# Optimization experiments

Hardware: AMD Instinct MI355X
Metric: run time of the kernel (lower is better)

## Reference

```python
import jax, jax.numpy as jnp
import numpy as np

N_NODES = 32768
N_EDGES = 196608
N_GRAPHS = 256
DEG = 6
HID = 128
RVD = 16
EMB = HID - RVD   # atom/bond embedding dim = hidden - random_vec_dim
VOCAB = 128
TGT = 256
DEPTH = 5
N_AGG = 4         # mean, max, min, std
N_SC = 3          # identity, amplification, attenuation
EPS = 1e-5


def setup_inputs() -> dict:
    key = jax.random.key(0)
    ks = jax.random.split(key, 12)

    def g(i, shape, scale=0.05):
        return jax.random.normal(ks[i], shape, dtype=jnp.float32) * scale

    return {
        "atom_feats": jax.random.randint(ks[0], (N_NODES, 9), 0, 100),
        "bond_feats": jax.random.randint(ks[1], (N_EDGES, 3), 0, 4),
        "src": jax.random.randint(ks[2], (N_EDGES,), 0, N_NODES),
        # every node receives exactly DEG messages (DGL reduce requires in-edges)
        "dst": jnp.repeat(jnp.arange(N_NODES), DEG),
        "graph_ids": jnp.repeat(jnp.arange(N_GRAPHS), N_NODES // N_GRAPHS),
        "n_graphs": N_GRAPHS,
        "rand_x": jax.random.normal(ks[3], (N_NODES, RVD), dtype=jnp.float32),   # std=1.0
        "rand_edge": jax.random.normal(ks[4], (N_EDGES, RVD), dtype=jnp.float32),
        "atom_emb": g(5, (9, VOCAB, EMB)),
        "bond_emb": g(6, (3, VOCAB, EMB)),
        "pre_W": g(7, (DEPTH, 3 * HID, HID)),
        "pre_b": jnp.zeros((DEPTH, HID), jnp.float32),
        "post_W": g(8, (DEPTH, (N_AGG * N_SC + 1) * HID, HID)),
        "post_b": jnp.zeros((DEPTH, HID), jnp.float32),
        "ro_W1": g(9, (3 * HID, HID)),
        "ro_b1": jnp.zeros((HID,), jnp.float32),
        "ro_W2": g(10, (HID, TGT)),
        "ro_b2": jnp.zeros((TGT,), jnp.float32),
    }


def reference(atom_feats, bond_feats, src, dst, graph_ids, n_graphs,
              rand_x, rand_edge, atom_emb, bond_emb,
              pre_W, pre_b, post_W, post_b, ro_W1, ro_b1, ro_W2, ro_b2):
    n = atom_feats.shape[0]
    # OGB-style encoders: sum of per-column embeddings, then concat random vec
    h = jnp.concatenate([atom_emb[jnp.arange(9), atom_feats].sum(1), rand_x], -1)   # [N, HID]
    ef = jnp.concatenate([bond_emb[jnp.arange(3), bond_feats].sum(1), rand_edge], -1)  # [E, HID]

    deg = jax.ops.segment_sum(jnp.ones((dst.shape[0],), h.dtype), dst, n)
    degc = jnp.maximum(deg, 1.0)[:, None]
    logD = jnp.log(deg + 1.0)[:, None]                 # avg_d['log'] = 1.0
    inv_logD = jnp.where(logD > 0, 1.0 / jnp.maximum(logD, EPS), 0.0)

    def layer(hc, p):
        pW, pb, qW, qb = p
        # pretrans MLP on [src_feat, dst_feat, edge_feat]; last_activation = activation (relu)
        z = jnp.concatenate([hc[src], hc[dst], ef], -1)          # [E, 3*HID]
        e = jax.nn.relu(z @ pW + pb)                             # [E, HID]
        s = jax.ops.segment_sum(e, dst, n)
        mean = s / degc
        mean_sq = jax.ops.segment_sum(e * e, dst, n) / degc
        mx = jax.ops.segment_max(e, dst, n)
        mn = jax.ops.segment_min(e, dst, n)
        std = jnp.sqrt(jax.nn.relu(mean_sq - mean * mean) + EPS)
        agg = jnp.concatenate([mean, mx, mn, std], -1)           # [N, 4*HID]
        scaled = jnp.concatenate([agg, agg * logD, agg * inv_logD], -1)  # [N, 12*HID]
        h_new = jnp.concatenate([hc, scaled], -1) @ qW + qb + hc  # posttrans (linear) + residual
        return h_new, None

    h, _ = jax.lax.scan(layer, h, (pre_W, pre_b, post_W, post_b))

    # multi-aggregator readout: mean, sum, max per graph
    cnt = jnp.maximum(jax.ops.segment_sum(jnp.ones((n,), h.dtype), graph_ids, n_graphs), 1.0)[:, None]
    gsum = jax.ops.segment_sum(h, graph_ids, n_graphs)
    gmax = jax.ops.segment_max(h, graph_ids, n_graphs)
    r = jnp.concatenate([gsum / cnt, gsum, gmax], -1)            # [G, 3*HID]
    return jax.nn.relu(r @ ro_W1 + ro_b1) @ ro_W2 + ro_b2        # [G, TGT]
```

## Files before the change

kernel.cpp:

```cpp
#include <hip/hip_runtime.h>
#include <hip/hip_bf16.h>

#define N_NODES 32768
#define N_EDGES 196608
#define N_GRAPHS 256
#define DEG 6
#define HID 128
#define RVD 16
#define EMB 112
#define VOCAB 128
#define TGT 256
#define DEPTH 5

#define LOG7 1.9459101090932196f
#define ILOG7 0.5138983423697507f

typedef __hip_bfloat16 bf16;
using frag_ab = __attribute__((ext_vector_type(8))) short;
using frag_cd = __attribute__((ext_vector_type(4))) float;
typedef float f32x2 __attribute__((ext_vector_type(2)));

static __device__ __forceinline__ float b2f(bf16 x) { return __bfloat162float(x); }
static __device__ __forceinline__ bf16  f2b(float x) { return __float2bfloat16(x); }
static __device__ __forceinline__ float us2f(unsigned short u) {
    unsigned int x = ((unsigned int)u) << 16;
    return __uint_as_float(x);
}
static __device__ __forceinline__ unsigned short f2us(float x) {
    bf16 b = __float2bfloat16(x);
    return *reinterpret_cast<unsigned short*>(&b);
}

#define PB_ENC  16384
#define PB_WB   (PB_ENC + 640)
#define PB_WC   (PB_WB + 1600)
#define PB_WR   (PB_WC + 80)
#define PB_CODE (PB_WR + 768)
#define PB_T    (PB_CODE + 320)

__global__ __launch_bounds__(256) void prep_k(const int* __restrict__ af, const float* __restrict__ rx,
                                              const float* __restrict__ aemb, bf16* __restrict__ h,
                                              const float* __restrict__ preW, const float* __restrict__ preB,
                                              const float* __restrict__ postW,
                                              const int* __restrict__ bfeat, const float* __restrict__ bemb,
                                              bf16* __restrict__ wb, bf16* __restrict__ wc,
                                              bf16* __restrict__ wrB, unsigned char* __restrict__ codeA,
                                              bf16* __restrict__ Tb) {
    int blk = blockIdx.x, tid = threadIdx.x;
    if (blk < PB_ENC) {
        int v = blk * 2 + (tid >> 7), c = tid & 127;
        float val;
        if (c < EMB) {
            val = 0.f;
            #pragma unroll
            for (int i = 0; i < 9; ++i) {
                int f = af[v * 9 + i];
                val += aemb[(i * VOCAB + f) * EMB + c];
            }
        } else {
            val = rx[v * RVD + (c - EMB)];
        }
        h[(size_t)v * HID + c] = f2b(val);
    } else if (blk < PB_WB) {
        int idx = (blk - PB_ENC) * 256 + tid;
        if (idx < DEPTH * 32768) {
            int j = idx & 7, L = (idx >> 3) & 63, nt = (idx >> 9) & 15, ks = (idx >> 13) & 3, l = idx >> 15;
            int k = ks * 32 + ((L >> 4) * 8) + j;
            int n = nt * 16 + (L & 15);
            const float* W = preW + (size_t)l * 384 * 128;
            float v = (n < 128) ? W[k * 128 + n] : W[(128 + k) * 128 + (n - 128)];
            wb[idx] = f2b(v);
        }
    } else if (blk < PB_WC) {
        int idx = (blk - PB_WB) * 256 + tid;
        if (idx < DEPTH * 81920) {
            int j = idx & 7, L = (idx >> 3) & 63, nt = (idx >> 9) & 7;
            int t = idx >> 12;
            int ks = t % 20, l = t / 20;
            int k = ks * 32 + ((L >> 4) * 8) + j;
            int n = nt * 16 + (L & 15);
            const float* W = postW + (size_t)l * 1664 * 128;
            float v;
            if (k < 128) {
                v = W[k * 128 + n];
            } else {
                int jj = k - 128;
                v = W[(128 + jj) * 128 + n] + LOG7 * W[(640 + jj) * 128 + n] + ILOG7 * W[(1152 + jj) * 128 + n];
            }
            wc[idx] = f2b(v);
        }
    } else if (blk < PB_WR) {
        int idx = (blk - PB_WC) * 256 + tid;
        if (idx < DEPTH * 4096) {
            int j = idx & 7, L = (idx >> 3) & 63, nt = (idx >> 9) & 7, l = idx >> 12;
            int k = ((L >> 4) * 8) + j;
            int n = nt * 16 + (L & 15);
            float v = (k < 16) ? preW[(size_t)l * 384 * 128 + (368 + k) * 128 + n] : 0.f;
            wrB[idx] = f2b(v);
        }
    } else if (blk < PB_CODE) {
        int e = (blk - PB_WR) * 256 + tid;
        if (e < N_EDGES)
            codeA[e] = (unsigned char)(bfeat[e * 3] | (bfeat[e * 3 + 1] << 2) | (bfeat[e * 3 + 2] << 4));
    } else {
        if (tid < 128) {
            int t = blk - PB_CODE;
            int l = t >> 6, cd = t & 63, c = tid;
            int f0 = cd & 3, f1 = (cd >> 2) & 3, f2 = cd >> 4;
            const float* W = preW + (size_t)l * 384 * 128 + 256 * 128;
            float acc = preB[l * 128 + c];
            #pragma unroll 4
            for (int k = 0; k < EMB; ++k) {
                float bsk = bemb[(0 * VOCAB + f0) * EMB + k]
                          + bemb[(1 * VOCAB + f1) * EMB + k]
                          + bemb[(2 * VOCAB + f2) * EMB + k];
                acc += bsk * W[k * 128 + c];
            }
            Tb[(size_t)(l * 64 + cd) * 128 + c] = f2b(acc);
        }
    }
}

__global__ __launch_bounds__(256) void gemm_z12(const bf16* __restrict__ A,
                                                const bf16* __restrict__ Bp,
                                                bf16* __restrict__ C) {
    int lane = threadIdx.x & 63;
    int wave = threadIdx.x >> 6;
    int m = lane & 15, quad = lane >> 4;
    int row0 = blockIdx.x * 64 + wave * 16;

    frag_cd acc[16];
    #pragma unroll
    for (int nt = 0; nt < 16; ++nt)
        #pragma unroll
        for (int i = 0; i < 4; ++i) acc[nt][i] = 0.f;

    const frag_ab* Bf = (const frag_ab*)Bp;
    const bf16* arow = A + (size_t)(row0 + m) * 128;
    #pragma unroll
    for (int ks = 0; ks < 4; ++ks) {
        frag_ab a = *(const frag_ab*)(arow + ks * 32 + quad * 8);
        #pragma unroll
        for (int nt = 0; nt < 16; ++nt) {
            frag_ab b = Bf[(ks * 16 + nt) * 64 + lane];
            acc[nt] = __builtin_amdgcn_mfma_f32_16x16x32_bf16(a, b, acc[nt], 0, 0, 0);
        }
    }
    #pragma unroll
    for (int nt = 0; nt < 16; ++nt) {
        int col = nt * 16 + m;
        #pragma unroll
        for (int r = 0; r < 4; ++r) {
            int row = row0 + quad * 4 + r;
            C[(size_t)row * 256 + col] = f2b(acc[nt][r]);
        }
    }
}

__global__ __launch_bounds__(512, 4) void fused_layer(bf16* __restrict__ h,
                                                      const bf16* __restrict__ Zcur,
                                                      const int* __restrict__ src,
                                                      const unsigned char* __restrict__ code,
                                                      const float* __restrict__ rand_edge,
                                                      const bf16* __restrict__ Tb,
                                                      const float* __restrict__ Wr,
                                                      const bf16* __restrict__ Bp,
                                                      const float* __restrict__ bias,
                                                      const bf16* __restrict__ Bn,
                                                      bf16* __restrict__ Znext) {
    __shared__ __align__(16) bf16 agg_lds[64 * 520];
    __shared__ __align__(16) float relds[8][384];

    int tid = threadIdx.x;
    int lane = tid & 63, wave = tid >> 6;
    int m = lane & 15, quad = lane >> 4;
    int row0 = blockIdx.x * 64;

    const unsigned short* Zu = (const unsigned short*)Zcur;
    const unsigned short* Tu = (const unsigned short*)Tb;
    unsigned short* Ag = (unsigned short*)agg_lds;
    int c = lane * 2;

    {
        const int vbase = row0 + wave * 8;

        f32x2 wr2[16];
        #pragma unroll
        for (int k = 0; k < 16; ++k) {
            float2 w2 = *(const float2*)(Wr + k * 128 + c);
            wr2[k].x = w2.x; wr2[k].y = w2.y;
        }

        {
            const float2* rb = (const float2*)(rand_edge + (size_t)vbase * 96);
            float2 a0 = rb[lane], a1 = rb[lane + 64], a2 = rb[lane + 128];
            float2* rl = (float2*)relds[wave];
            rl[lane] = a0; rl[lane + 64] = a1; rl[lane + 128] = a2;
        }
        float2 rh0, rh1, rh2;

        int svs[2][6]; int cds[2][6];
        ushort2 z1u[2][6], tvu[2][6], z2u[2];

        {
            const int2* sp = (const int2*)(src + vbase * 6);
            int2 a = sp[0], b = sp[1], d = sp[2];
            svs[0][0] = a.x; svs[0][1] = a.y; svs[0][2] = b.x;
            svs[0][3] = b.y; svs[0][4] = d.x; svs[0][5] = d.y;
            const unsigned short* cp = (const unsigned short*)(code + vbase * 6);
            unsigned short x = cp[0], y = cp[1], z = cp[2];
            cds[0][0] = x & 255; cds[0][1] = x >> 8; cds[0][2] = y & 255;
            cds[0][3] = y >> 8;  cds[0][4] = z & 255; cds[0][5] = z >> 8;
        }
        z2u[0] = *(const ushort2*)(Zu + (size_t)vbase * 256 + 128 + c);
        #pragma unroll
        for (int j = 0; j < 6; ++j) z1u[0][j] = *(const ushort2*)(Zu + (size_t)svs[0][j] * 256 + c);
        #pragma unroll
        for (int j = 0; j < 6; ++j) tvu[0][j] = *(const ushort2*)(Tu + cds[0][j] * 128 + c);
        {
            const int2* sp = (const int2*)(src + (vbase + 1) * 6);
            int2 a = sp[0], b = sp[1], d = sp[2];
            svs[1][0] = a.x; svs[1][1] = a.y; svs[1][2] = b.x;
            svs[1][3] = b.y; svs[1][4] = d.x; svs[1][5] = d.y;
            const unsigned short* cp = (const unsigned short*)(code + (vbase + 1) * 6);
            unsigned short x = cp[0], y = cp[1], z = cp[2];
            cds[1][0] = x & 255; cds[1][1] = x >> 8; cds[1][2] = y & 255;
            cds[1][3] = y >> 8;  cds[1][4] = z & 255; cds[1][5] = z >> 8;
        }

        #pragma unroll
        for (int i = 0; i < 8; ++i) {
            const int s = i & 1, t = s ^ 1;
            if (i == 2) {
                const float2* rb2 = (const float2*)(rand_edge + (size_t)(vbase + 4) * 96);
                rh0 = rb2[lane]; rh1 = rb2[lane + 64]; rh2 = rb2[lane + 128];
            }
            if (i == 4) {
                float2* rl = (float2*)relds[wave];
                rl[lane] = rh0; rl[lane + 64] = rh1; rl[lane + 128] = rh2;
            }
            if (i < 7) {
                z2u[t] = *(const ushort2*)(Zu + (size_t)(vbase + i + 1) * 256 + 128 + c);
                #pragma unroll
                for (int j = 0; j < 6; ++j) z1u[t][j] = *(const ushort2*)(Zu + (size_t)svs[t][j] * 256 + c);
                #pragma unroll
                for (int j = 0; j < 6; ++j) tvu[t][j] = *(const ushort2*)(Tu + cds[t][j] * 128 + c);
            }
            if (i < 6) {
                const int2* sp = (const int2*)(src + (vbase + i + 2) * 6);
                int2 a = sp[0], b = sp[1], d = sp[2];
                svs[s][0] = a.x; svs[s][1] = a.y; svs[s][2] = b.x;
                svs[s][3] = b.y; svs[s][4] = d.x; svs[s][5] = d.y;
                const unsigned short* cp = (const unsigned short*)(code + (vbase + i + 2) * 6);
                unsigned short x = cp[0], y = cp[1], z = cp[2];
                cds[s][0] = x & 255; cds[s][1] = x >> 8; cds[s][2] = y & 255;
                cds[s][3] = y >> 8;  cds[s][4] = z & 255; cds[s][5] = z >> 8;
            }

            float z2a = us2f(z2u[s].x), z2b = us2f(z2u[s].y);
            f32x2 s2  = {0.f, 0.f}, ss2 = {0.f, 0.f};
            f32x2 mx2 = {-1e30f, -1e30f}, mn2 = {1e30f, 1e30f};
            #pragma unroll
            for (int j = 0; j < 6; ++j) {
                const float4* rp = (const float4*)&relds[wave][(i & 3) * 96 + j * 16];
                float4 r0 = rp[0], r1 = rp[1], r2 = rp[2], r3 = rp[3];
                f32x2 v2;
                v2.x = us2f(z1u[s][j].x) + z2a + us2f(tvu[s][j].x);
                v2.y = us2f(z1u[s][j].y) + z2b + us2f(tvu[s][j].y);
                float rk[16] = {r0.x, r0.y, r0.z, r0.w, r1.x, r1.y, r1.z, r1.w,
                                r2.x, r2.y, r2.z, r2.w, r3.x, r3.y, r3.z, r3.w};
                #pragma unroll
                for (int k = 0; k < 16; ++k) v2 += rk[k] * wr2[k];
                v2 = __builtin_elementwise_max(v2, (f32x2){0.f, 0.f});
                s2 += v2;
                ss2 += v2 * v2;
                mx2 = __builtin_elementwise_max(mx2, v2);
                mn2 = __builtin_elementwise_min(mn2, v2);
            }
            f32x2 mean2 = s2 * (1.f / 6.f);
            f32x2 msq2  = ss2 * (1.f / 6.f);
            f32x2 var2  = __builtin_elementwise_max(msq2 - mean2 * mean2, (f32x2){0.f, 0.f});
            float sda = sqrtf(var2.x + 1e-5f), sdb = sqrtf(var2.y + 1e-5f);
            int lrow = wave * 8 + i;
            size_t base = (size_t)lrow * 520 + c;
            *(ushort2*)(Ag + base)       = make_ushort2(f2us(mean2.x), f2us(mean2.y));
            *(ushort2*)(Ag + base + 128) = make_ushort2(f2us(mx2.x),   f2us(mx2.y));
            *(ushort2*)(Ag + base + 256) = make_ushort2(f2us(mn2.x),   f2us(mn2.y));
            *(ushort2*)(Ag + base + 384) = make_ushort2(f2us(sda),     f2us(sdb));
        }
    }
    __syncthreads();

    int rt = wave & 3, nh = wave >> 2;
    int rowA = row0 + rt * 16 + m;

    frag_cd acc[4];
    #pragma unroll
    for (int nt = 0; nt < 4; ++nt)
        #pragma unroll
        for (int i = 0; i < 4; ++i) acc[nt][i] = 0.f;

    const frag_ab* Bf = (const frag_ab*)Bp;
    const bf16* arow = h + (size_t)rowA * 128;
    #pragma unroll
    for (int ks = 0; ks < 4; ++ks) {
        frag_ab a = *(const frag_ab*)(arow + ks * 32 + quad * 8);
        #pragma unroll
        for (int nt = 0; nt < 4; ++nt) {
            frag_ab b = Bf[(ks * 8 + nh * 4 + nt) * 64 + lane];
            acc[nt] = __builtin_amdgcn_mfma_f32_16x16x32_bf16(a, b, acc[nt], 0, 0, 0);
        }
    }
    const bf16* grow = agg_lds + (size_t)(rt * 16 + m) * 520;
    #pragma unroll
    for (int ks = 0; ks < 16; ++ks) {
        frag_ab a = *(const frag_ab*)(grow + ks * 32 + quad * 8);
        #pragma unroll
        for (int nt = 0; nt < 4; ++nt) {
            frag_ab b = Bf[((4 + ks) * 8 + nh * 4 + nt) * 64 + lane];
            acc[nt] = __builtin_amdgcn_mfma_f32_16x16x32_bf16(a, b, acc[nt], 0, 0, 0);
        }
    }

    __syncthreads();

    bf16* newh = agg_lds;
    #pragma unroll
    for (int nt = 0; nt < 4; ++nt) {
        int col = nh * 64 + nt * 16 + m;
        float bs_ = bias[col];
        #pragma unroll
        for (int r2 = 0; r2 < 4; ++r2) {
            int lr = rt * 16 + quad * 4 + r2;
            int row = row0 + lr;
            float nv = acc[nt][r2] + bs_ + b2f(h[(size_t)row * HID + col]);
            bf16 bv2 = f2b(nv);
            h[(size_t)row * HID + col] = bv2;
            newh[lr * 136 + col] = bv2;
        }
    }

    if (Bn) {
        __syncthreads();
        const frag_ab* Bf2 = (const frag_ab*)Bn;
        frag_cd a2[8];
        #pragma unroll
        for (int nt = 0; nt < 8; ++nt)
            #pragma unroll
            for (int i = 0; i < 4; ++i) a2[nt][i] = 0.f;
        #pragma unroll
        for (int ks = 0; ks < 4; ++ks) {
            frag_ab a = *(const frag_ab*)&newh[(rt * 16 + m) * 136 + ks * 32 + quad * 8];
            #pragma unroll
            for (int nt = 0; nt < 8; ++nt) {
                frag_ab b = Bf2[(ks * 16 + nh * 8 + nt) * 64 + lane];
                a2[nt] = __builtin_amdgcn_mfma_f32_16x16x32_bf16(a, b, a2[nt], 0, 0, 0);
            }
        }
        #pragma unroll
        for (int nt = 0; nt < 8; ++nt) {
            int col = nh * 128 + nt * 16 + m;
            #pragma unroll
            for (int r2 = 0; r2 < 4; ++r2) {
                int row = row0 + rt * 16 + quad * 4 + r2;
                Znext[(size_t)row * 256 + col] = f2b(a2[nt][r2]);
            }
        }
    }
}

__global__ __launch_bounds__(128) void readout(const bf16* __restrict__ h, const float* __restrict__ W1,
                                               const float* __restrict__ b1, const float* __restrict__ W2,
                                               const float* __restrict__ b2, float* __restrict__ out) {
    __shared__ float r[384];
    __shared__ float y1[128];
    int g = blockIdx.x, c = threadIdx.x;
    float s = 0.f, mx = -1e30f;
    for (int v = 0; v < 128; ++v) {
        float hv = b2f(h[((size_t)g * 128 + v) * HID + c]);
        s += hv; mx = fmaxf(mx, hv);
    }
    r[c] = s * (1.f / 128.f);
    r[128 + c] = s;
    r[256 + c] = mx;
    __syncthreads();
    float a1 = b1[c];
    for (int k = 0; k < 384; ++k) a1 += r[k] * W1[k * 128 + c];
    y1[c] = fmaxf(a1, 0.f);
    __syncthreads();
    #pragma unroll
    for (int o = 0; o < 2; ++o) {
        int t = c + o * 128;
        float a2 = b2[t];
        for (int k = 0; k < 128; ++k) a2 += y1[k] * W2[k * 256 + t];
        out[(size_t)g * 256 + t] = a2;
    }
}

extern "C" void kernel_launch(void* const* d_in, const int* in_sizes, int n_in,
                              void* d_out, int out_size, void* d_ws, size_t ws_size,
                              hipStream_t stream) {
    const int*   atom_feats = (const int*)d_in[0];
    const int*   bond_feats = (const int*)d_in[1];
    const int*   src        = (const int*)d_in[2];
    const float* rand_x     = (const float*)d_in[6];
    const float* rand_edge  = (const float*)d_in[7];
    const float* atom_emb   = (const float*)d_in[8];
    const float* bond_emb   = (const float*)d_in[9];
    const float* pre_W      = (const float*)d_in[10];
    const float* pre_b      = (const float*)d_in[11];
    const float* post_W     = (const float*)d_in[12];
    const float* post_b     = (const float*)d_in[13];
    const float* ro_W1      = (const float*)d_in[14];
    const float* ro_b1      = (const float*)d_in[15];
    const float* ro_W2      = (const float*)d_in[16];
    const float* ro_b2      = (const float*)d_in[17];

    char* p = (char*)d_ws;
    auto alloc = [&](size_t bytes) {
        char* r = p;
        p += (bytes + 255) & ~(size_t)255;
        return r;
    };
    bf16*  h    = (bf16*) alloc((size_t)N_NODES * HID * 2);
    bf16*  z12a = (bf16*) alloc((size_t)N_NODES * 256 * 2);
    bf16*  z12b = (bf16*) alloc((size_t)N_NODES * 256 * 2);
    bf16*  wb   = (bf16*) alloc((size_t)DEPTH * 32768 * 2);
    bf16*  wc   = (bf16*) alloc((size_t)DEPTH * 81920 * 2);
    bf16*  wrB  = (bf16*) alloc((size_t)DEPTH * 4096 * 2);
    bf16*  Tb   = (bf16*) alloc((size_t)DEPTH * 64 * 128 * 2);
    unsigned char* code = (unsigned char*)alloc(N_EDGES);

    prep_k<<<PB_T, 256, 0, stream>>>(atom_feats, rand_x, atom_emb, h,
                                     pre_W, pre_b, post_W,
                                     bond_feats, bond_emb,
                                     wb, wc, wrB, code, Tb);

    gemm_z12<<<N_NODES / 64, 256, 0, stream>>>(h, wb, z12a);

    bf16* zc = z12a;
    bf16* zn = z12b;
    for (int l = 0; l < DEPTH; ++l) {
        const bf16* wbn = (l + 1 < DEPTH) ? (wb + (size_t)(l + 1) * 32768) : nullptr;
        fused_layer<<<N_NODES / 64, 512, 0, stream>>>(
            h, zc, src, code, rand_edge,
            Tb + (size_t)l * 8192,
            pre_W + (size_t)l * 384 * 128 + 368 * 128,
            wc + (size_t)l * 81920,
            post_b + l * HID,
            wbn, zn);
        bf16* t = zc; zc = zn; zn = t;
    }

    readout<<<N_GRAPHS, 128, 0, stream>>>(h, ro_W1, ro_b1, ro_W2, ro_b2, (float*)d_out);
}
```

Measured before the change: 337.7 us.

## Deepen gather prefetch to triple buffer and retile MFMA waves 2x2

The neighbor-gather loop moves from double to triple buffering: gathers run two nodes ahead and index loads four nodes ahead, which hides more global-load latency. The post-transform and next-layer GEMMs are retiled so each wave computes a 2x2 block of 16x16 tiles (two row tiles times two or four column tiles) instead of one row tile times four or eight column tiles. Each B fragment loaded from global memory is now reused across two row tiles, which roughly halves B-weight traffic per wave. The cost is more registers from the extra gather buffer and the larger accumulator block, which could lower occupancy under the 512x4 launch bounds.

```diff
diff --git a/kernel.cpp b/kernel.cpp
--- a/kernel.cpp
+++ b/kernel.cpp
@@ -173,7 +173,7 @@
 
     int tid = threadIdx.x;
     int lane = tid & 63, wave = tid >> 6;
-    int m = lane & 15, quad = lane >> 4;
+    int ml = lane & 15, quad = lane >> 4;
     int row0 = blockIdx.x * 64;
 
     const unsigned short* Zu = (const unsigned short*)Zcur;
@@ -200,37 +200,40 @@
         float2 rh0, rh1, rh2;
 
         int svs[2][6]; int cds[2][6];
-        ushort2 z1u[2][6], tvu[2][6], z2u[2];
-
-        {
-            const int2* sp = (const int2*)(src + vbase * 6);
-            int2 a = sp[0], b = sp[1], d = sp[2];
-            svs[0][0] = a.x; svs[0][1] = a.y; svs[0][2] = b.x;
-            svs[0][3] = b.y; svs[0][4] = d.x; svs[0][5] = d.y;
-            const unsigned short* cp = (const unsigned short*)(code + vbase * 6);
-            unsigned short x = cp[0], y = cp[1], z = cp[2];
-            cds[0][0] = x & 255; cds[0][1] = x >> 8; cds[0][2] = y & 255;
-            cds[0][3] = y >> 8;  cds[0][4] = z & 255; cds[0][5] = z >> 8;
-        }
-        z2u[0] = *(const ushort2*)(Zu + (size_t)vbase * 256 + 128 + c);
-        #pragma unroll
-        for (int j = 0; j < 6; ++j) z1u[0][j] = *(const ushort2*)(Zu + (size_t)svs[0][j] * 256 + c);
-        #pragma unroll
-        for (int j = 0; j < 6; ++j) tvu[0][j] = *(const ushort2*)(Tu + cds[0][j] * 128 + c);
-        {
-            const int2* sp = (const int2*)(src + (vbase + 1) * 6);
-            int2 a = sp[0], b = sp[1], d = sp[2];
-            svs[1][0] = a.x; svs[1][1] = a.y; svs[1][2] = b.x;
-            svs[1][3] = b.y; svs[1][4] = d.x; svs[1][5] = d.y;
-            const unsigned short* cp = (const unsigned short*)(code + (vbase + 1) * 6);
-            unsigned short x = cp[0], y = cp[1], z = cp[2];
-            cds[1][0] = x & 255; cds[1][1] = x >> 8; cds[1][2] = y & 255;
-            cds[1][3] = y >> 8;  cds[1][4] = z & 255; cds[1][5] = z >> 8;
-        }
+        ushort2 z1u[3][6], tvu[3][6], z2u[3];
+
+#define LOADIDX(node, slot)                                                        \
+        {                                                                          \
+            const int2* sp = (const int2*)(src + (size_t)(vbase + (node)) * 6);    \
+            int2 a_ = sp[0], b_ = sp[1], d_ = sp[2];                               \
+            svs[slot][0] = a_.x; svs[slot][1] = a_.y; svs[slot][2] = b_.x;         \
+            svs[slot][3] = b_.y; svs[slot][4] = d_.x; svs[slot][5] = d_.y;         \
+            const unsigned short* cp = (const unsigned short*)(code + (vbase + (node)) * 6); \
+            unsigned short x_ = cp[0], y_ = cp[1], z_ = cp[2];                     \
+            cds[slot][0] = x_ & 255; cds[slot][1] = x_ >> 8; cds[slot][2] = y_ & 255; \
+            cds[slot][3] = y_ >> 8;  cds[slot][4] = z_ & 255; cds[slot][5] = z_ >> 8; \
+        }
+
+#define GATHER(node, gs, is)                                                       \
+        {                                                                          \
+            z2u[gs] = *(const ushort2*)(Zu + (size_t)(vbase + (node)) * 256 + 128 + c); \
+            _Pragma("unroll")                                                      \
+            for (int j = 0; j < 6; ++j)                                            \
+                z1u[gs][j] = *(const ushort2*)(Zu + (size_t)svs[is][j] * 256 + c); \
+            _Pragma("unroll")                                                      \
+            for (int j = 0; j < 6; ++j)                                            \
+                tvu[gs][j] = *(const ushort2*)(Tu + cds[is][j] * 128 + c);         \
+        }
+
+        LOADIDX(0, 0); LOADIDX(1, 1);
+        GATHER(0, 0, 0);
+        LOADIDX(2, 0);
+        GATHER(1, 1, 1);
+        LOADIDX(3, 1);
 
         #pragma unroll
         for (int i = 0; i < 8; ++i) {
-            const int s = i & 1, t = s ^ 1;
+            const int s = i % 3;
             if (i == 2) {
                 const float2* rb2 = (const float2*)(rand_edge + (size_t)(vbase + 4) * 96);
                 rh0 = rb2[lane]; rh1 = rb2[lane + 64]; rh2 = rb2[lane + 128];
@@ -239,23 +242,8 @@
                 float2* rl = (float2*)relds[wave];
                 rl[lane] = rh0; rl[lane + 64] = rh1; rl[lane + 128] = rh2;
             }
-            if (i < 7) {
-                z2u[t] = *(const ushort2*)(Zu + (size_t)(vbase + i + 1) * 256 + 128 + c);
-                #pragma unroll
-                for (int j = 0; j < 6; ++j) z1u[t][j] = *(const ushort2*)(Zu + (size_t)svs[t][j] * 256 + c);
-                #pragma unroll
-                for (int j = 0; j < 6; ++j) tvu[t][j] = *(const ushort2*)(Tu + cds[t][j] * 128 + c);
-            }
-            if (i < 6) {
-                const int2* sp = (const int2*)(src + (vbase + i + 2) * 6);
-                int2 a = sp[0], b = sp[1], d = sp[2];
-                svs[s][0] = a.x; svs[s][1] = a.y; svs[s][2] = b.x;
-                svs[s][3] = b.y; svs[s][4] = d.x; svs[s][5] = d.y;
-                const unsigned short* cp = (const unsigned short*)(code + (vbase + i + 2) * 6);
-                unsigned short x = cp[0], y = cp[1], z = cp[2];
-                cds[s][0] = x & 255; cds[s][1] = x >> 8; cds[s][2] = y & 255;
-                cds[s][3] = y >> 8;  cds[s][4] = z & 255; cds[s][5] = z >> 8;
-            }
+            if (i < 6) GATHER(i + 2, (i + 2) % 3, i & 1);
+            if (i < 4) LOADIDX(i + 4, i & 1);
 
             float z2a = us2f(z2u[s].x), z2b = us2f(z2u[s].y);
             f32x2 s2  = {0.f, 0.f}, ss2 = {0.f, 0.f};
@@ -288,37 +276,44 @@
             *(ushort2*)(Ag + base + 256) = make_ushort2(f2us(mn2.x),   f2us(mn2.y));
             *(ushort2*)(Ag + base + 384) = make_ushort2(f2us(sda),     f2us(sdb));
         }
+#undef LOADIDX
+#undef GATHER
     }
     __syncthreads();
 
-    int rt = wave & 3, nh = wave >> 2;
-    int rowA = row0 + rt * 16 + m;
-
-    frag_cd acc[4];
-    #pragma unroll
-    for (int nt = 0; nt < 4; ++nt)
-        #pragma unroll
-        for (int i = 0; i < 4; ++i) acc[nt][i] = 0.f;
+    int mh = wave >> 2, ng = wave & 3;
+
+    frag_cd acc[2][2];
+    #pragma unroll
+    for (int m2 = 0; m2 < 2; ++m2)
+        #pragma unroll
+        for (int nt = 0; nt < 2; ++nt)
+            #pragma unroll
+            for (int i = 0; i < 4; ++i) acc[m2][nt][i] = 0.f;
 
     const frag_ab* Bf = (const frag_ab*)Bp;
-    const bf16* arow = h + (size_t)rowA * 128;
     #pragma unroll
     for (int ks = 0; ks < 4; ++ks) {
-        frag_ab a = *(const frag_ab*)(arow + ks * 32 + quad * 8);
-        #pragma unroll
-        for (int nt = 0; nt < 4; ++nt) {
-            frag_ab b = Bf[(ks * 8 + nh * 4 + nt) * 64 + lane];
-            acc[nt] = __builtin_amdgcn_mfma_f32_16x16x32_bf16(a, b, acc[nt], 0, 0, 0);
-        }
-    }
-    const bf16* grow = agg_lds + (size_t)(rt * 16 + m) * 520;
+        frag_ab b0 = Bf[(ks * 8 + ng * 2 + 0) * 64 + lane];
+        frag_ab b1 = Bf[(ks * 8 + ng * 2 + 1) * 64 + lane];
+        #pragma unroll
+        for (int m2 = 0; m2 < 2; ++m2) {
+            int mt = mh * 2 + m2;
+            frag_ab a = *(const frag_ab*)(h + (size_t)(row0 + mt * 16 + ml) * 128 + ks * 32 + quad * 8);
+            acc[m2][0] = __builtin_amdgcn_mfma_f32_16x16x32_bf16(a, b0, acc[m2][0], 0, 0, 0);
+            acc[m2][1] = __builtin_amdgcn_mfma_f32_16x16x32_bf16(a, b1, acc[m2][1], 0, 0, 0);
+        }
+    }
     #pragma unroll
     for (int ks = 0; ks < 16; ++ks) {
-        frag_ab a = *(const frag_ab*)(grow + ks * 32 + quad * 8);
-        #pragma unroll
-        for (int nt = 0; nt < 4; ++nt) {
-            frag_ab b = Bf[((4 + ks) * 8 + nh * 4 + nt) * 64 + lane];
-            acc[nt] = __builtin_amdgcn_mfma_f32_16x16x32_bf16(a, b, acc[nt], 0, 0, 0);
+        frag_ab b0 = Bf[((4 + ks) * 8 + ng * 2 + 0) * 64 + lane];
+        frag_ab b1 = Bf[((4 + ks) * 8 + ng * 2 + 1) * 64 + lane];
+        #pragma unroll
+        for (int m2 = 0; m2 < 2; ++m2) {
+            int mt = mh * 2 + m2;
+            frag_ab a = *(const frag_ab*)(agg_lds + (size_t)(mt * 16 + ml) * 520 + ks * 32 + quad * 8);
+            acc[m2][0] = __builtin_amdgcn_mfma_f32_16x16x32_bf16(a, b0, acc[m2][0], 0, 0, 0);
+            acc[m2][1] = __builtin_amdgcn_mfma_f32_16x16x32_bf16(a, b1, acc[m2][1], 0, 0, 0);
         }
     }
 
@@ -326,44 +321,58 @@
 
     bf16* newh = agg_lds;
     #pragma unroll
-    for (int nt = 0; nt < 4; ++nt) {
-        int col = nh * 64 + nt * 16 + m;
+    for (int nt = 0; nt < 2; ++nt) {
+        int col = (ng * 2 + nt) * 16 + ml;
         float bs_ = bias[col];
         #pragma unroll
-        for (int r2 = 0; r2 < 4; ++r2) {
-            int lr = rt * 16 + quad * 4 + r2;
-            int row = row0 + lr;
-            float nv = acc[nt][r2] + bs_ + b2f(h[(size_t)row * HID + col]);
-            bf16 bv2 = f2b(nv);
-            h[(size_t)row * HID + col] = bv2;
-            newh[lr * 136 + col] = bv2;
+        for (int m2 = 0; m2 < 2; ++m2) {
+            #pragma unroll
+            for (int r2 = 0; r2 < 4; ++r2) {
+                int lr = (mh * 2 + m2) * 16 + quad * 4 + r2;
+                int row = row0 + lr;
+                float nv = acc[m2][nt][r2] + bs_ + b2f(h[(size_t)row * HID + col]);
+                bf16 bv2 = f2b(nv);
+                h[(size_t)row * HID + col] = bv2;
+                newh[lr * 136 + col] = bv2;
+            }
         }
     }
 
     if (Bn) {
         __syncthreads();
         const frag_ab* Bf2 = (const frag_ab*)Bn;
-        frag_cd a2[8];
-        #pragma unroll
-        for (int nt = 0; nt < 8; ++nt)
-            #pragma unroll
-            for (int i = 0; i < 4; ++i) a2[nt][i] = 0.f;
+        frag_cd a2[2][4];
+        #pragma unroll
+        for (int m2 = 0; m2 < 2; ++m2)
+            #pragma unroll
+            for (int nt = 0; nt < 4; ++nt)
+                #pragma unroll
+                for (int i = 0; i < 4; ++i) a2[m2][nt][i] = 0.f;
         #pragma unroll
         for (int ks = 0; ks < 4; ++ks) {
-            frag_ab a = *(const frag_ab*)&newh[(rt * 16 + m) * 136 + ks * 32 + quad * 8];
-            #pragma unroll
-            for (int nt = 0; nt < 8; ++nt) {
-                frag_ab b = Bf2[(ks * 16 + nh * 8 + nt) * 64 + lane];
-                a2[nt] = __builtin_amdgcn_mfma_f32_16x16x32_bf16(a, b, a2[nt], 0, 0, 0);
-            }
-        }
-        #pragma unroll
-        for (int nt = 0; nt < 8; ++nt) {
-            int col = nh * 128 + nt * 16 + m;
-            #pragma unroll
-            for (int r2 = 0; r2 < 4; ++r2) {
-                int row = row0 + rt * 16 + quad * 4 + r2;
-                Znext[(size_t)row * 256 + col] = f2b(a2[nt][r2]);
+            frag_ab bb[4];
+            #pragma unroll
+            for (int nt = 0; nt < 4; ++nt)
+                bb[nt] = Bf2[(ks * 16 + ng * 4 + nt) * 64 + lane];
+            #pragma unroll
+            for (int m2 = 0; m2 < 2; ++m2) {
+                int mt = mh * 2 + m2;
+                frag_ab a = *(const frag_ab*)&newh[(mt * 16 + ml) * 136 + ks * 32 + quad * 8];
+                #pragma unroll
+                for (int nt = 0; nt < 4; ++nt)
+                    a2[m2][nt] = __builtin_amdgcn_mfma_f32_16x16x32_bf16(a, bb[nt], a2[m2][nt], 0, 0, 0);
+            }
+        }
+        #pragma unroll
+        for (int m2 = 0; m2 < 2; ++m2) {
+            #pragma unroll
+            for (int nt = 0; nt < 4; ++nt) {
+                int col = (ng * 4 + nt) * 16 + ml;
+                #pragma unroll
+                for (int r2 = 0; r2 < 4; ++r2) {
+                    int row = row0 + (mh * 2 + m2) * 16 + quad * 4 + r2;
+                    Znext[(size_t)row * 256 + col] = f2b(a2[m2][nt][r2]);
+                }
             }
         }
     }
```

New measurement: 333.2 us. Within noise of the previous version (-1.3%).

## Retile layer GEMMs to 2x2 wave blocks and stage outputs through LDS

Applied to the files above, without the earlier changes.

Wave work in the fused layer GEMMs changes from one 16-row tile by four column tiles to two row tiles by two (or four) column tiles. Each B fragment loaded from global memory is now reused across two row tiles, which cuts B-matrix traffic per wave. The residual update and the Znext output are staged through LDS so they can be written with coalesced 16-byte vector stores instead of scattered 2-byte stores. The cost is extra LDS round trips and barriers, and register pressure rises slightly.

```diff
diff --git a/kernel.cpp b/kernel.cpp
--- a/kernel.cpp
+++ b/kernel.cpp
@@ -173,7 +173,7 @@
 
     int tid = threadIdx.x;
     int lane = tid & 63, wave = tid >> 6;
-    int m = lane & 15, quad = lane >> 4;
+    int ml = lane & 15, quad = lane >> 4;
     int row0 = blockIdx.x * 64;
 
     const unsigned short* Zu = (const unsigned short*)Zcur;
@@ -291,81 +291,130 @@
     }
     __syncthreads();
 
-    int rt = wave & 3, nh = wave >> 2;
-    int rowA = row0 + rt * 16 + m;
-
-    frag_cd acc[4];
-    #pragma unroll
-    for (int nt = 0; nt < 4; ++nt)
-        #pragma unroll
-        for (int i = 0; i < 4; ++i) acc[nt][i] = 0.f;
+    int mh = wave >> 2, ng = wave & 3;
+
+    frag_cd acc[2][2];
+    #pragma unroll
+    for (int m2 = 0; m2 < 2; ++m2)
+        #pragma unroll
+        for (int nt = 0; nt < 2; ++nt)
+            #pragma unroll
+            for (int i = 0; i < 4; ++i) acc[m2][nt][i] = 0.f;
 
     const frag_ab* Bf = (const frag_ab*)Bp;
-    const bf16* arow = h + (size_t)rowA * 128;
     #pragma unroll
     for (int ks = 0; ks < 4; ++ks) {
-        frag_ab a = *(const frag_ab*)(arow + ks * 32 + quad * 8);
-        #pragma unroll
-        for (int nt = 0; nt < 4; ++nt) {
-            frag_ab b = Bf[(ks * 8 + nh * 4 + nt) * 64 + lane];
-            acc[nt] = __builtin_amdgcn_mfma_f32_16x16x32_bf16(a, b, acc[nt], 0, 0, 0);
-        }
-    }
-    const bf16* grow = agg_lds + (size_t)(rt * 16 + m) * 520;
+        frag_ab b0 = Bf[(ks * 8 + ng * 2 + 0) * 64 + lane];
+        frag_ab b1 = Bf[(ks * 8 + ng * 2 + 1) * 64 + lane];
+        #pragma unroll
+        for (int m2 = 0; m2 < 2; ++m2) {
+            int mt = mh * 2 + m2;
+            frag_ab a = *(const frag_ab*)(h + (size_t)(row0 + mt * 16 + ml) * 128 + ks * 32 + quad * 8);
+            acc[m2][0] = __builtin_amdgcn_mfma_f32_16x16x32_bf16(a, b0, acc[m2][0], 0, 0, 0);
+            acc[m2][1] = __builtin_amdgcn_mfma_f32_16x16x32_bf16(a, b1, acc[m2][1], 0, 0, 0);
+        }
+    }
     #pragma unroll
     for (int ks = 0; ks < 16; ++ks) {
-        frag_ab a = *(const frag_ab*)(grow + ks * 32 + quad * 8);
-        #pragma unroll
-        for (int nt = 0; nt < 4; ++nt) {
-            frag_ab b = Bf[((4 + ks) * 8 + nh * 4 + nt) * 64 + lane];
-            acc[nt] = __builtin_amdgcn_mfma_f32_16x16x32_bf16(a, b, acc[nt], 0, 0, 0);
+        frag_ab b0 = Bf[((4 + ks) * 8 + ng * 2 + 0) * 64 + lane];
+        frag_ab b1 = Bf[((4 + ks) * 8 + ng * 2 + 1) * 64 + lane];
+        #pragma unroll
+        for (int m2 = 0; m2 < 2; ++m2) {
+            int mt = mh * 2 + m2;
+            frag_ab a = *(const frag_ab*)(agg_lds + (size_t)(mt * 16 + ml) * 520 + ks * 32 + quad * 8);
+            acc[m2][0] = __builtin_amdgcn_mfma_f32_16x16x32_bf16(a, b0, acc[m2][0], 0, 0, 0);
+            acc[m2][1] = __builtin_amdgcn_mfma_f32_16x16x32_bf16(a, b1, acc[m2][1], 0, 0, 0);
         }
     }
 
     __syncthreads();
 
-    bf16* newh = agg_lds;
-    #pragma unroll
-    for (int nt = 0; nt < 4; ++nt) {
-        int col = nh * 64 + nt * 16 + m;
+    float* pgemm = (float*)agg_lds;
+    #pragma unroll
+    for (int nt = 0; nt < 2; ++nt) {
+        int col = (ng * 2 + nt) * 16 + ml;
         float bs_ = bias[col];
         #pragma unroll
-        for (int r2 = 0; r2 < 4; ++r2) {
-            int lr = rt * 16 + quad * 4 + r2;
-            int row = row0 + lr;
-            float nv = acc[nt][r2] + bs_ + b2f(h[(size_t)row * HID + col]);
-            bf16 bv2 = f2b(nv);
-            h[(size_t)row * HID + col] = bv2;
-            newh[lr * 136 + col] = bv2;
-        }
+        for (int m2 = 0; m2 < 2; ++m2) {
+            #pragma unroll
+            for (int r2 = 0; r2 < 4; ++r2) {
+                int lr = (mh * 2 + m2) * 16 + quad * 4 + r2;
+                pgemm[lr * 132 + col] = acc[m2][nt][r2] + bs_;
+            }
+        }
+    }
+    __syncthreads();
+
+    bf16* newh = agg_lds + 16896;
+    {
+        int row = tid >> 3, cg = tid & 7;
+        const float4* pg = (const float4*)(pgemm + row * 132 + cg * 16);
+        float4 p0 = pg[0], p1 = pg[1], p2 = pg[2], p3 = pg[3];
+        unsigned short* hrow = (unsigned short*)(h + (size_t)(row0 + row) * 128 + cg * 16);
+        frag_ab h0 = *(const frag_ab*)hrow;
+        frag_ab h1 = *(const frag_ab*)(hrow + 8);
+        float nv[16] = {p0.x, p0.y, p0.z, p0.w, p1.x, p1.y, p1.z, p1.w,
+                        p2.x, p2.y, p2.z, p2.w, p3.x, p3.y, p3.z, p3.w};
+        #pragma unroll
+        for (int j = 0; j < 8; ++j) nv[j]     += us2f((unsigned short)h0[j]);
+        #pragma unroll
+        for (int j = 0; j < 8; ++j) nv[8 + j] += us2f((unsigned short)h1[j]);
+        frag_ab o0, o1;
+        #pragma unroll
+        for (int j = 0; j < 8; ++j) o0[j] = (short)f2us(nv[j]);
+        #pragma unroll
+        for (int j = 0; j < 8; ++j) o1[j] = (short)f2us(nv[8 + j]);
+        *(frag_ab*)hrow = o0;
+        *(frag_ab*)(hrow + 8) = o1;
+        *(frag_ab*)&newh[row * 136 + cg * 16] = o0;
+        *(frag_ab*)&newh[row * 136 + cg * 16 + 8] = o1;
     }
 
     if (Bn) {
         __syncthreads();
         const frag_ab* Bf2 = (const frag_ab*)Bn;
-        frag_cd a2[8];
-        #pragma unroll
-        for (int nt = 0; nt < 8; ++nt)
-            #pragma unroll
-            for (int i = 0; i < 4; ++i) a2[nt][i] = 0.f;
+        frag_cd a2[2][4];
+        #pragma unroll
+        for (int m2 = 0; m2 < 2; ++m2)
+            #pragma unroll
+            for (int nt = 0; nt < 4; ++nt)
+                #pragma unroll
+                for (int i = 0; i < 4; ++i) a2[m2][nt][i] = 0.f;
         #pragma unroll
         for (int ks = 0; ks < 4; ++ks) {
-            frag_ab a = *(const frag_ab*)&newh[(rt * 16 + m) * 136 + ks * 32 + quad * 8];
-            #pragma unroll
-            for (int nt = 0; nt < 8; ++nt) {
-                frag_ab b = Bf2[(ks * 16 + nh * 8 + nt) * 64 + lane];
-                a2[nt] = __builtin_amdgcn_mfma_f32_16x16x32_bf16(a, b, a2[nt], 0, 0, 0);
-            }
-        }
-        #pragma unroll
-        for (int nt = 0; nt < 8; ++nt) {
-            int col = nh * 128 + nt * 16 + m;
-            #pragma unroll
-            for (int r2 = 0; r2 < 4; ++r2) {
-                int row = row0 + rt * 16 + quad * 4 + r2;
-                Znext[(size_t)row * 256 + col] = f2b(a2[nt][r2]);
-            }
-        }
+            frag_ab bb[4];
+            #pragma unroll
+            for (int nt = 0; nt < 4; ++nt)
+                bb[nt] = Bf2[(ks * 16 + ng * 4 + nt) * 64 + lane];
+            #pragma unroll
+            for (int m2 = 0; m2 < 2; ++m2) {
+                int mt = mh * 2 + m2;
+                frag_ab a = *(const frag_ab*)&newh[(mt * 16 + ml) * 136 + ks * 32 + quad * 8];
+                #pragma unroll
+                for (int nt = 0; nt < 4; ++nt)
+                    a2[m2][nt] = __builtin_amdgcn_mfma_f32_16x16x32_bf16(a, bb[nt], a2[m2][nt], 0, 0, 0);
+            }
+        }
+        bf16* ztile = agg_lds;
+        #pragma unroll
+        for (int m2 = 0; m2 < 2; ++m2) {
+            #pragma unroll
+            for (int nt = 0; nt < 4; ++nt) {
+                int col = (ng * 4 + nt) * 16 + ml;
+                #pragma unroll
+                for (int r2 = 0; r2 < 4; ++r2) {
+                    int lr = (mh * 2 + m2) * 16 + quad * 4 + r2;
+                    ztile[lr * 264 + col] = f2b(a2[m2][nt][r2]);
+                }
+            }
+        }
+        __syncthreads();
+        int row = tid >> 3, cg = tid & 7;
+        unsigned short* zr = (unsigned short*)(Znext + (size_t)(row0 + row) * 256 + cg * 32);
+        const unsigned short* zs = (const unsigned short*)ztile + row * 264 + cg * 32;
+        #pragma unroll
+        for (int k2 = 0; k2 < 4; ++k2)
+            *(frag_ab*)(zr + k2 * 8) = *(const frag_ab*)(zs + k2 * 8);
     }
 }
 
```

Result: no change. 334.1 us (-1.1%).
